# Optimization experiments

Hardware: AMD Instinct MI355X
Metric: run time of the kernel (lower is better)

Reference implementation:

```python
import jax, jax.numpy as jnp
import numpy as np
from jax import lax

KERNEL = 3      # patch size
STRIDE = 1      # matching stride at low res
RATE = 2        # downsample rate
SOFTMAX_SCALE = 10.0


def _extract_patches(img, k, stride):
    """tf.image.extract_patches with SAME padding. img: [B,H,W,C] -> [B, oh*ow, k, k, C]."""
    B, H, W, C = img.shape
    oh = -(-H // stride)
    ow = -(-W // stride)
    ph = max((oh - 1) * stride + k - H, 0)
    pw = max((ow - 1) * stride + k - W, 0)
    img = jnp.pad(img, ((0, 0), (ph // 2, ph - ph // 2), (pw // 2, pw - pw // 2), (0, 0)))
    # stack the k*k shifted strided views; channel-last order matches TF's (kh, kw, C) flattening
    cols = [img[:, dh:dh + (oh - 1) * stride + 1:stride, dw:dw + (ow - 1) * stride + 1:stride, :]
            for dh in range(k) for dw in range(k)]
    p = jnp.stack(cols, axis=3)  # [B, oh, ow, k*k, C]
    return p.reshape(B, oh * ow, k, k, C)


def _avgpool2(x):
    """Exact equivalent of TF bilinear (antialias=False) downsample by factor 2."""
    B, H, W, C = x.shape
    return x.reshape(B, H // 2, 2, W // 2, 2, C).mean(axis=(2, 4))


def _conv_same(x4, w):
    return lax.conv_general_dilated(x4, w, (1, 1), 'SAME',
                                    dimension_numbers=('NHWC', 'HWIO', 'NHWC'))


def _forward(x, mask):
    B, H, W, C = x.shape
    k, stride, rate = KERNEL, STRIDE, RATE
    h, w = H // rate, W // rate
    L = h * w

    # raw (full-res) patches used for reconstruction: [B,k,k,C,L]
    raw_w = jnp.transpose(_extract_patches(x, k, rate * stride), (0, 2, 3, 4, 1))
    # low-res foreground / background (identical here, as in the source)
    f = _avgpool2(x)              # [B,h,w,C]
    m = _avgpool2(mask)           # [B,h,w,1]
    # low-res matching patches: [B,k,k,C,L]
    wp = jnp.transpose(_extract_patches(f, k, stride), (0, 2, 3, 4, 1))
    # mask patches -> gate: mm = 1 where the 3x3 mask patch mean is exactly 1.0
    mp = _extract_patches(m, k, stride)                       # [B,L,k,k,1]
    mm = (jnp.mean(mp, axis=(2, 3, 4)) == 1.0).astype(jnp.float32)  # [B,L]

    fuse_w = jnp.eye(KERNEL, dtype=jnp.float32).reshape(KERNEL, KERNEL, 1, 1)

    def per_item(xi, wi, rwi, mmi):
        # xi:[h,w,C]  wi,rwi:[k,k,C,L]  mmi:[L]
        wn = wi / jnp.maximum(jnp.sqrt(jnp.sum(wi * wi, axis=(0, 1, 2))), 1e-4)
        yi = _conv_same(xi[None], wn)          # [1,h,w,L] cosine-similarity logits
        att = yi[0]
        # fuse: diagonal conv over the [L,L] score matrix in both patch orderings
        z = yi.reshape(1, L, L, 1)
        z = _conv_same(z, fuse_w)
        z = z.reshape(1, h, w, h, w).transpose(0, 2, 1, 4, 3).reshape(1, L, L, 1)
        z = _conv_same(z, fuse_w)
        z = z.reshape(1, w, h, w, h).transpose(0, 2, 1, 4, 3)
        yi = z.reshape(1, h, w, L)
        mm4 = mmi.reshape(1, 1, 1, L)
        yi = jax.nn.softmax(yi * mm4 * SOFTMAX_SCALE, axis=3) * mm4
        # reconstruction: transposed conv with raw full-res patches as filters
        out = lax.conv_transpose(yi, rwi, (rate, rate), 'SAME',
                                 dimension_numbers=('NHWC', 'HWIO', 'NHWC'),
                                 transpose_kernel=True) / float(rate * rate)
        return out[0], att

    y, att = jax.vmap(per_item)(f, wp, raw_w, mm)
    return y, att


def setup_inputs() -> dict:
    key = jax.random.key(0)
    x = jax.random.normal(key, (2, 128, 128, 64), dtype=jnp.float32)
    # binary hole mask: ones inside a centered 64x64 square
    mask = jnp.zeros((2, 128, 128, 1), jnp.float32).at[:, 32:96, 32:96, :].set(1.0)
    return {"x": x, "mask": mask}


def reference(x, mask):
    return _forward(x, mask)
```

## Files before the change

### kernel.cpp

```cpp
#include <hip/hip_runtime.h>
#include <hip/hip_bf16.h>

typedef _Float16 f16x8 __attribute__((ext_vector_type(8)));
typedef float f32x4 __attribute__((ext_vector_type(4)));

__device__ __forceinline__ void gload_lds16(const void* gptr, void* lptr) {
  __builtin_amdgcn_global_load_lds(
      (const __attribute__((address_space(1))) void*)gptr,
      (__attribute__((address_space(3))) void*)lptr, 16, 0, 0);
}

__global__ __launch_bounds__(256) void k_prt(const float* __restrict__ x,
                                             const float* __restrict__ mask,
                                             _Float16* __restrict__ f_h,
                                             float* __restrict__ sumsq,
                                             float* __restrict__ mlow,
                                             _Float16* __restrict__ Rt,
                                             float* __restrict__ y) {
  if (blockIdx.x < 2048) {
    int wave = threadIdx.x >> 6, c = threadIdx.x & 63;
    int blk = blockIdx.x * 4 + wave;
    int b = blk >> 12, ij = blk & 4095;
    int i = ij >> 6, j = ij & 63;
    size_t base = ((size_t)(b * 128 + 2 * i) * 128 + 2 * j) * 64 + c;
    float f = 0.25f * (x[base] + x[base + 64] + x[base + 128 * 64] + x[base + 128 * 64 + 64]);
    f_h[(size_t)blk * 64 + c] = (_Float16)f;
    float fsq = f * f;
    for (int off = 32; off; off >>= 1) fsq += __shfl_down(fsq, off);
    if (c == 0) {
      sumsq[blk] = fsq;
      size_t mb = (size_t)(b * 128 + 2 * i) * 128 + 2 * j;
      mlow[blk] = 0.25f * (mask[mb] + mask[mb + 1] + mask[mb + 128] + mask[mb + 129]);
    }
    return;
  }
  if (blockIdx.x >= 2432) {
    int idx = blockIdx.x - 2432;
    f32x4* Y4 = (f32x4*)y;
    f32x4 z = {0.f, 0.f, 0.f, 0.f};
#pragma unroll
    for (int k = 0; k < 4; ++k) Y4[idx * 1024 + k * 256 + threadIdx.x] = z;
    return;
  }
  int idx = blockIdx.x - 2048;
  int kh = idx % 3;
  int rest = idx / 3;
  int li = rest & 63, b = rest >> 6;
  int r = 2 * li + kh;
  __shared__ float xrow[128 * 65];
  if (r < 128) {
    for (int t = threadIdx.x; t < 8192; t += 256) {
      int v = t >> 6, c = t & 63;
      xrow[v * 65 + c] = x[((size_t)(b * 128 + r) * 128 + v) * 64 + c];
    }
  }
  __syncthreads();
  for (int id2 = threadIdx.x; id2 < 12288; id2 += 256) {
    int lj = id2 & 63, rest2 = id2 >> 6;
    int c = rest2 & 63, kw = rest2 >> 6;
    int v = 2 * lj + kw;
    float val = (r < 128 && v < 128) ? xrow[v * 65 + c] : 0.f;
    int n = (kh * 3 + kw) * 64 + c;
    Rt[((size_t)b * 640 + n) * 4096 + li * 64 + lj] = (_Float16)val;
  }
}

__global__ __launch_bounds__(1024) void k_norm_compact(const float* __restrict__ sumsq,
                                                       const float* __restrict__ mlow,
                                                       float* __restrict__ invn,
                                                       int* __restrict__ actIdx,
                                                       int* __restrict__ nAct) {
  int b = blockIdx.x;
  int t = threadIdx.x;
  __shared__ unsigned char mmf[4096];
  for (int l = t; l < 4096; l += 1024) {
    int li = l >> 6, lj = l & 63;
    float s = 0.f;
    bool ok = true;
    for (int dh = -1; dh <= 1; ++dh)
      for (int dw = -1; dw <= 1; ++dw) {
        int ii = li + dh, jj = lj + dw;
        float mv = 0.f;
        if ((unsigned)ii < 64u && (unsigned)jj < 64u) {
          int idx = (b << 12) + ii * 64 + jj;
          s += sumsq[idx];
          mv = mlow[idx];
        }
        ok = ok && (mv == 1.0f);
      }
    invn[(b << 12) + l] = 1.0f / fmaxf(sqrtf(s), 1e-4f);
    mmf[l] = ok ? 1 : 0;
  }
  __syncthreads();
  int lane = t & 63, wv = t >> 6;
  __shared__ int wsum[16];
  __shared__ int sbase;
  if (t == 0) sbase = 0;
  __syncthreads();
  for (int chunk = 0; chunk < 4; ++chunk) {
    int l = chunk * 1024 + t;
    int flag = mmf[l] ? 1 : 0;
    unsigned long long m = __ballot(flag);
    int wpre = __popcll(m & ((1ull << lane) - 1ull));
    if (lane == 0) wsum[wv] = __popcll(m);
    __syncthreads();
    int off = sbase;
    for (int w2 = 0; w2 < wv; ++w2) off += wsum[w2];
    if (flag) {
      int pos = off + wpre;
      if (pos < 1024) actIdx[(b << 10) + pos] = l;
    }
    __syncthreads();
    if (t == 0) {
      int s2 = 0;
      for (int w2 = 0; w2 < 16; ++w2) s2 += wsum[w2];
      sbase += s2;
    }
    __syncthreads();
  }
  int total = sbase;
  if (t >= total) actIdx[(b << 10) + t] = 0;
  if (t == 0) nAct[b] = (total > 1024) ? 1024 : total;
}

__global__ __launch_bounds__(256) void k_psub(const _Float16* __restrict__ f_h,
                                              _Float16* __restrict__ P,
                                              const _Float16* __restrict__ Rt,
                                              const int* __restrict__ actIdx,
                                              _Float16* __restrict__ Rts) {
  if (blockIdx.x < 2048) {
    int wave = threadIdx.x >> 6, c = threadIdx.x & 63;
    int blk = blockIdx.x * 4 + wave;
    int b = blk >> 12, l = blk & 4095;
    int li = l >> 6, lj = l & 63;
    _Float16* dst = P + (size_t)blk * 576 + c;
#pragma unroll
    for (int kk = 0; kk < 9; ++kk) {
      int kh = kk / 3, kw = kk % 3;
      int ii = li + kh - 1, jj = lj + kw - 1;
      _Float16 v = (_Float16)0.f;
      if ((unsigned)ii < 64u && (unsigned)jj < 64u)
        v = f_h[((size_t)(b << 12) + ii * 64 + jj) * 64 + c];
      dst[kk * 64] = v;
    }
    return;
  }
  int idx = blockIdx.x - 2048;
  int n = idx % 640, b = idx / 640;
  const unsigned short* src = (const unsigned short*)(Rt + ((size_t)b * 640 + n) * 4096);
  _Float16* dst = Rts + ((size_t)b * 640 + n) * 1024;
  const int* aIdx = actIdx + (b << 10);
  int s0 = threadIdx.x * 4;
  unsigned long long v = (unsigned long long)src[aIdx[s0]] |
                         ((unsigned long long)src[aIdx[s0 + 1]] << 16) |
                         ((unsigned long long)src[aIdx[s0 + 2]] << 32) |
                         ((unsigned long long)src[aIdx[s0 + 3]] << 48);
  *(unsigned long long*)(dst + s0) = v;
}

__global__ __launch_bounds__(256) void k_gemm_sim(const _Float16* __restrict__ P,
                                                  const float* __restrict__ invn,
                                                  float* __restrict__ att) {
  int b = blockIdx.z;
  const _Float16* Ab = P + (size_t)b * 4096 * 576;
  int idx0 = blockIdx.x;
  int idx = (idx0 & 7) * 66 + (idx0 >> 3);
  int bj = (int)((sqrtf(8.f * (float)idx + 1.f) - 1.f) * 0.5f);
  while ((bj + 1) * (bj + 2) / 2 <= idx) ++bj;
  while (bj * (bj + 1) / 2 > idx) --bj;
  int bi = idx - bj * (bj + 1) / 2;
  int rowBase = bi * 128, colBase = bj * 128;
  bool diag = (bi == bj);

  __shared__ alignas(16) _Float16 As[128 * 64];
  __shared__ alignas(16) _Float16 Bs[128 * 64];
  __shared__ alignas(16) float tbuf[32][132];
  int tid = threadIdx.x, wave = tid >> 6, lane = tid & 63;
  int q = lane >> 4, rr = lane & 15;
  int wr = (wave >> 1) * 64, wc = (wave & 1) * 64;
  f32x4 acc[4][4] = {};
  for (int kt = 0; kt < 576; kt += 64) {
    __syncthreads();
#pragma unroll
    for (int t = 0; t < 4; ++t) {
      int chunk = t * 256 + wave * 64 + lane;
      int row = chunk >> 3;
      int kc = ((chunk & 7) ^ (row & 7)) * 8;
      gload_lds16(Ab + (size_t)(rowBase + row) * 576 + kt + kc,
                  As + (size_t)(t * 256 + wave * 64) * 8);
      if (!diag)
        gload_lds16(Ab + (size_t)(colBase + row) * 576 + kt + kc,
                    Bs + (size_t)(t * 256 + wave * 64) * 8);
    }
    __syncthreads();
    const _Float16* Bsrc = diag ? As : Bs;
#pragma unroll
    for (int ks = 0; ks < 2; ++ks) {
      f16x8 af[4], bf[4];
#pragma unroll
      for (int mi = 0; mi < 4; ++mi) {
        int r = wr + mi * 16 + rr;
        int ps = (ks * 4 + q) ^ (r & 7);
        af[mi] = *(const f16x8*)(As + r * 64 + ps * 8);
      }
#pragma unroll
      for (int ni = 0; ni < 4; ++ni) {
        int r = wc + ni * 16 + rr;
        int ps = (ks * 4 + q) ^ (r & 7);
        bf[ni] = *(const f16x8*)(Bsrc + r * 64 + ps * 8);
      }
#pragma unroll
      for (int mi = 0; mi < 4; ++mi)
#pragma unroll
        for (int ni = 0; ni < 4; ++ni)
          acc[mi][ni] = __builtin_amdgcn_mfma_f32_16x16x32_f16(af[mi], bf[ni], acc[mi][ni], 0, 0, 0);
    }
  }
  float* attb = att + ((size_t)b << 24);
#pragma unroll
  for (int ni = 0; ni < 4; ++ni) {
    int gc = colBase + wc + ni * 16 + rr;
    float sc = invn[(b << 12) + gc];
#pragma unroll
    for (int mi = 0; mi < 4; ++mi)
#pragma unroll
      for (int reg = 0; reg < 4; ++reg) {
        int gr = rowBase + wr + mi * 16 + q * 4 + reg;
        attb[((size_t)gr << 12) + gc] = acc[mi][ni][reg] * sc;
      }
  }
  if (diag) return;
  const float* ivrow = invn + (b << 12) + rowBase;
#pragma unroll
  for (int ph = 0; ph < 4; ++ph) {
    __syncthreads();
    if ((ph >> 1) == (wc >> 6)) {
      int nlo = (ph & 1) * 2;
#pragma unroll
      for (int nn = 0; nn < 2; ++nn) {
        int ni = nlo + nn;
        int rloc = nn * 16 + rr;
#pragma unroll
        for (int mi = 0; mi < 4; ++mi)
          *(f32x4*)&tbuf[rloc][wr + mi * 16 + q * 4] = acc[mi][ni];
      }
    }
    __syncthreads();
    int r = tid >> 3;
    int cbase = (tid & 7) * 16;
    int grow = colBase + ph * 32 + r;
    float* dst = attb + ((size_t)grow << 12) + rowBase + cbase;
#pragma unroll
    for (int cc = 0; cc < 16; cc += 4) {
      f32x4 v = *(f32x4*)&tbuf[r][cbase + cc];
      f32x4 s = *(const f32x4*)(ivrow + cbase + cc);
      *(f32x4*)(dst + cc) = v * s;
    }
  }
}

__global__ __launch_bounds__(256) void k_fuse_softmax3(const float* __restrict__ att,
                                                       const int* __restrict__ actIdx,
                                                       const int* __restrict__ nAct,
                                                       _Float16* __restrict__ Asub) {
  int blk0 = blockIdx.x;
  int blk = (blk0 & 7) * 1024 + (blk0 >> 3);
  int b = blk >> 12, p = blk & 4095;
  const float* Y = att + ((size_t)b << 24);
  const int* aIdx = actIdx + (b << 10);
  int na = nAct[b];
  int tid = threadIdx.x;
  int pi = p >> 6, pj = p & 63;
  int acol = pj * 64 + pi;

  int ls[4];
  bool act[4];
  float F[4] = {0.f, 0.f, 0.f, 0.f};
#pragma unroll
  for (int s4 = 0; s4 < 4; ++s4) {
    int slot = s4 * 256 + tid;
    ls[s4] = aIdx[slot];
    act[s4] = (slot < na);
  }

#pragma unroll
  for (int d2 = -1; d2 <= 1; ++d2) {
    int a2 = acol + d2;
    if ((unsigned)a2 >= 4096u) continue;
    int p2 = ((a2 & 63) << 6) | (a2 >> 6);
    int l2[4];
    bool lok[4];
#pragma unroll
    for (int s4 = 0; s4 < 4; ++s4) {
      int l = ls[s4];
      int bcol = ((l & 63) << 6) | (l >> 6);
      int b2 = bcol + d2;
      lok[s4] = act[s4] && ((unsigned)b2 < 4096u);
      int b2c = lok[s4] ? b2 : 0;
      l2[s4] = ((b2c & 63) << 6) | (b2c >> 6);
    }
#pragma unroll
    for (int d1 = -1; d1 <= 1; ++d1) {
      int qq = p2 + d1;
      if ((unsigned)qq >= 4096u) continue;
      const float* row = Y + ((size_t)qq << 12);
#pragma unroll
      for (int s4 = 0; s4 < 4; ++s4) {
        int rr2 = l2[s4] + d1;
        if (lok[s4] && (unsigned)rr2 < 4096u) F[s4] += row[rr2];
      }
    }
  }

  float z[4];
  float mx = (na < 4096) ? 0.f : -1e30f;
#pragma unroll
  for (int s4 = 0; s4 < 4; ++s4) {
    z[s4] = act[s4] ? F[s4] * 10.f : -1e30f;
    mx = fmaxf(mx, z[s4]);
  }
  __shared__ float red[4];
  for (int off = 32; off; off >>= 1) mx = fmaxf(mx, __shfl_down(mx, off));
  if ((tid & 63) == 0) red[tid >> 6] = mx;
  __syncthreads();
  mx = fmaxf(fmaxf(red[0], red[1]), fmaxf(red[2], red[3]));
  float e[4];
  float esum = 0.f;
#pragma unroll
  for (int s4 = 0; s4 < 4; ++s4) {
    e[s4] = act[s4] ? __expf(z[s4] - mx) : 0.f;
    esum += e[s4];
  }
  for (int off = 32; off; off >>= 1) esum += __shfl_down(esum, off);
  __syncthreads();
  if ((tid & 63) == 0) red[tid >> 6] = esum;
  __syncthreads();
  float total = red[0] + red[1] + red[2] + red[3] + (float)(4096 - na) * __expf(0.f - mx);
  float inv = 1.f / total;
  _Float16* Ap = Asub + ((size_t)blk << 10);
#pragma unroll
  for (int s4 = 0; s4 < 4; ++s4) Ap[s4 * 256 + tid] = (_Float16)(e[s4] * inv);
}

__global__ __launch_bounds__(256) void k_gemm_recon(const _Float16* __restrict__ Asub,
                                                    const _Float16* __restrict__ Rts,
                                                    const int* __restrict__ nAct,
                                                    float* __restrict__ y) {
  int b = blockIdx.z;
  const _Float16* Ab = Asub + ((size_t)b << 22);
  const _Float16* Bb = Rts + (size_t)b * 640 * 1024;
  int kMax = ((nAct[b] + 63) >> 6) << 6;
  int rowBase = blockIdx.y * 128, colBase = blockIdx.x * 128;
  __shared__ alignas(16) _Float16 As[128 * 64];
  __shared__ alignas(16) _Float16 Bs[128 * 64];
  int tid = threadIdx.x, wave = tid >> 6, lane = tid & 63;
  int q = lane >> 4, rr = lane & 15;
  int wr = (wave >> 1) * 64, wc = (wave & 1) * 64;
  f32x4 acc[4][4] = {};
  for (int kt = 0; kt < kMax; kt += 64) {
    __syncthreads();
#pragma unroll
    for (int t = 0; t < 4; ++t) {
      int chunk = t * 256 + wave * 64 + lane;
      int row = chunk >> 3;
      int kc = ((chunk & 7) ^ (row & 7)) * 8;
      gload_lds16(Ab + ((size_t)(rowBase + row) << 10) + kt + kc,
                  As + (size_t)(t * 256 + wave * 64) * 8);
      gload_lds16(Bb + ((size_t)(colBase + row) << 10) + kt + kc,
                  Bs + (size_t)(t * 256 + wave * 64) * 8);
    }
    __syncthreads();
#pragma unroll
    for (int ks = 0; ks < 2; ++ks) {
      f16x8 af[4], bf[4];
#pragma unroll
      for (int mi = 0; mi < 4; ++mi) {
        int r = wr + mi * 16 + rr;
        int ps = (ks * 4 + q) ^ (r & 7);
        af[mi] = *(const f16x8*)(As + r * 64 + ps * 8);
      }
#pragma unroll
      for (int ni = 0; ni < 4; ++ni) {
        int r = wc + ni * 16 + rr;
        int ps = (ks * 4 + q) ^ (r & 7);
        bf[ni] = *(const f16x8*)(Bs + r * 64 + ps * 8);
      }
#pragma unroll
      for (int mi = 0; mi < 4; ++mi)
#pragma unroll
        for (int ni = 0; ni < 4; ++ni)
          acc[mi][ni] = __builtin_amdgcn_mfma_f32_16x16x32_f16(af[mi], bf[ni], acc[mi][ni], 0, 0, 0);
    }
  }
#pragma unroll
  for (int ni = 0; ni < 4; ++ni) {
    int gc = colBase + wc + ni * 16 + rr;
    if (gc < 576) {
      int kk = gc >> 6, c = gc & 63;
      int kh = kk / 3, kw = kk - kh * 3;
#pragma unroll
      for (int mi = 0; mi < 4; ++mi)
#pragma unroll
        for (int reg = 0; reg < 4; ++reg) {
          int gp = rowBase + wr + mi * 16 + q * 4 + reg;
          int i = gp >> 6, j = gp & 63;
          int u = 2 * i + kh, v = 2 * j + kw;
          if (u < 128 && v < 128)
            atomicAdd(y + (((size_t)((b * 128 + u) * 128 + v)) << 6) + c,
                      0.25f * acc[mi][ni][reg]);
        }
    }
  }
}

extern "C" void kernel_launch(void* const* d_in, const int* in_sizes, int n_in,
                              void* d_out, int out_size, void* d_ws, size_t ws_size,
                              hipStream_t stream) {
  const float* x = (const float*)d_in[0];
  const float* mask = (const float*)d_in[1];
  float* out = (float*)d_out;
  float* y = out;
  float* att = out + 2097152;

  char* ws = (char*)d_ws;
  _Float16* f_h = (_Float16*)(ws + 0);
  float* sumsq = (float*)(ws + 0x100000);
  float* mlow = (float*)(ws + 0x108000);
  float* invn = (float*)(ws + 0x110000);
  _Float16* P = (_Float16*)(ws + 0x120000);
  _Float16* Rt = (_Float16*)(ws + 0xA20000);
  int* actIdx = (int*)(ws + 0x1420000);
  int* nAct = (int*)(ws + 0x1422000);
  _Float16* Rts = (_Float16*)(ws + 0x1430000);
  _Float16* Asub = (_Float16*)(ws + 0x16B0000);
  (void)in_sizes; (void)n_in; (void)out_size; (void)ws_size;

  k_prt<<<2944, 256, 0, stream>>>(x, mask, f_h, sumsq, mlow, Rt, y);
  k_norm_compact<<<2, 1024, 0, stream>>>(sumsq, mlow, invn, actIdx, nAct);
  k_psub<<<3328, 256, 0, stream>>>(f_h, P, Rt, actIdx, Rts);
  k_gemm_sim<<<dim3(528, 1, 2), 256, 0, stream>>>(P, invn, att);
  k_fuse_softmax3<<<8192, 256, 0, stream>>>(att, actIdx, nAct, Asub);
  k_gemm_recon<<<dim3(5, 32, 2), 256, 0, stream>>>(Asub, Rts, nAct, y);
}
```

Baseline: 294.0 us.

## Gather raw patches directly from input and move norm computation into psub

Removes the full-size transposed raw-patch intermediate and instead gathers only the active patch columns directly from x when building the compacted reconstruction matrix. The inverse-norm computation is moved out of the two-block compaction kernel into extra parallel blocks of the gather kernel. This removes a large intermediate write and its read, at the cost of scattered, less coalesced reads from x.

```diff
diff --git a/kernel.cpp b/kernel.cpp
--- a/kernel.cpp
+++ b/kernel.cpp
@@ -15,7 +15,6 @@
                                              _Float16* __restrict__ f_h,
                                              float* __restrict__ sumsq,
                                              float* __restrict__ mlow,
-                                             _Float16* __restrict__ Rt,
                                              float* __restrict__ y) {
   if (blockIdx.x < 2048) {
     int wave = threadIdx.x >> 6, c = threadIdx.x & 63;
@@ -34,40 +33,14 @@
     }
     return;
   }
-  if (blockIdx.x >= 2432) {
-    int idx = blockIdx.x - 2432;
-    f32x4* Y4 = (f32x4*)y;
-    f32x4 z = {0.f, 0.f, 0.f, 0.f};
-#pragma unroll
-    for (int k = 0; k < 4; ++k) Y4[idx * 1024 + k * 256 + threadIdx.x] = z;
-    return;
-  }
   int idx = blockIdx.x - 2048;
-  int kh = idx % 3;
-  int rest = idx / 3;
-  int li = rest & 63, b = rest >> 6;
-  int r = 2 * li + kh;
-  __shared__ float xrow[128 * 65];
-  if (r < 128) {
-    for (int t = threadIdx.x; t < 8192; t += 256) {
-      int v = t >> 6, c = t & 63;
-      xrow[v * 65 + c] = x[((size_t)(b * 128 + r) * 128 + v) * 64 + c];
-    }
-  }
-  __syncthreads();
-  for (int id2 = threadIdx.x; id2 < 12288; id2 += 256) {
-    int lj = id2 & 63, rest2 = id2 >> 6;
-    int c = rest2 & 63, kw = rest2 >> 6;
-    int v = 2 * lj + kw;
-    float val = (r < 128 && v < 128) ? xrow[v * 65 + c] : 0.f;
-    int n = (kh * 3 + kw) * 64 + c;
-    Rt[((size_t)b * 640 + n) * 4096 + li * 64 + lj] = (_Float16)val;
-  }
-}
-
-__global__ __launch_bounds__(1024) void k_norm_compact(const float* __restrict__ sumsq,
-                                                       const float* __restrict__ mlow,
-                                                       float* __restrict__ invn,
+  f32x4* Y4 = (f32x4*)y;
+  f32x4 z = {0.f, 0.f, 0.f, 0.f};
+#pragma unroll
+  for (int k = 0; k < 4; ++k) Y4[idx * 1024 + k * 256 + threadIdx.x] = z;
+}
+
+__global__ __launch_bounds__(1024) void k_norm_compact(const float* __restrict__ mlow,
                                                        int* __restrict__ actIdx,
                                                        int* __restrict__ nAct) {
   int b = blockIdx.x;
@@ -75,20 +48,14 @@
   __shared__ unsigned char mmf[4096];
   for (int l = t; l < 4096; l += 1024) {
     int li = l >> 6, lj = l & 63;
-    float s = 0.f;
     bool ok = true;
     for (int dh = -1; dh <= 1; ++dh)
       for (int dw = -1; dw <= 1; ++dw) {
         int ii = li + dh, jj = lj + dw;
         float mv = 0.f;
-        if ((unsigned)ii < 64u && (unsigned)jj < 64u) {
-          int idx = (b << 12) + ii * 64 + jj;
-          s += sumsq[idx];
-          mv = mlow[idx];
-        }
+        if ((unsigned)ii < 64u && (unsigned)jj < 64u) mv = mlow[(b << 12) + ii * 64 + jj];
         ok = ok && (mv == 1.0f);
       }
-    invn[(b << 12) + l] = 1.0f / fmaxf(sqrtf(s), 1e-4f);
     mmf[l] = ok ? 1 : 0;
   }
   __syncthreads();
@@ -125,9 +92,11 @@
 
 __global__ __launch_bounds__(256) void k_psub(const _Float16* __restrict__ f_h,
                                               _Float16* __restrict__ P,
-                                              const _Float16* __restrict__ Rt,
+                                              const float* __restrict__ x,
                                               const int* __restrict__ actIdx,
-                                              _Float16* __restrict__ Rts) {
+                                              _Float16* __restrict__ Rts,
+                                              const float* __restrict__ sumsq,
+                                              float* __restrict__ invn) {
   if (blockIdx.x < 2048) {
     int wave = threadIdx.x >> 6, c = threadIdx.x & 63;
     int blk = blockIdx.x * 4 + wave;
@@ -145,16 +114,37 @@
     }
     return;
   }
+  if (blockIdx.x >= 3200) {
+    int t = (blockIdx.x - 3200) * 256 + threadIdx.x;
+    int b = t >> 12, l = t & 4095;
+    int li = l >> 6, lj = l & 63;
+    float s = 0.f;
+    for (int dh = -1; dh <= 1; ++dh)
+      for (int dw = -1; dw <= 1; ++dw) {
+        int ii = li + dh, jj = lj + dw;
+        if ((unsigned)ii < 64u && (unsigned)jj < 64u) s += sumsq[(b << 12) + ii * 64 + jj];
+      }
+    invn[t] = 1.0f / fmaxf(sqrtf(s), 1e-4f);
+    return;
+  }
   int idx = blockIdx.x - 2048;
-  int n = idx % 640, b = idx / 640;
-  const unsigned short* src = (const unsigned short*)(Rt + ((size_t)b * 640 + n) * 4096);
-  _Float16* dst = Rts + ((size_t)b * 640 + n) * 1024;
+  int n = idx % 576, b = idx / 576;
+  int kk = n >> 6, c = n & 63;
+  int kh = kk / 3, kw = kk - kh * 3;
+  _Float16* dst = Rts + ((size_t)(b * 640 + n) << 10);
   const int* aIdx = actIdx + (b << 10);
+  const float* xb = x + ((size_t)b << 20);
   int s0 = threadIdx.x * 4;
-  unsigned long long v = (unsigned long long)src[aIdx[s0]] |
-                         ((unsigned long long)src[aIdx[s0 + 1]] << 16) |
-                         ((unsigned long long)src[aIdx[s0 + 2]] << 32) |
-                         ((unsigned long long)src[aIdx[s0 + 3]] << 48);
+  unsigned long long v = 0;
+#pragma unroll
+  for (int u4 = 0; u4 < 4; ++u4) {
+    int l = aIdx[s0 + u4];
+    int li = l >> 6, lj = l & 63;
+    int r = 2 * li + kh, vv = 2 * lj + kw;
+    float val = (r < 128 && vv < 128) ? xb[((size_t)(r * 128 + vv) << 6) + c] : 0.f;
+    _Float16 h = (_Float16)val;
+    v |= ((unsigned long long)*(unsigned short*)&h) << (16 * u4);
+  }
   *(unsigned long long*)(dst + s0) = v;
 }
 
@@ -428,16 +418,15 @@
   float* mlow = (float*)(ws + 0x108000);
   float* invn = (float*)(ws + 0x110000);
   _Float16* P = (_Float16*)(ws + 0x120000);
-  _Float16* Rt = (_Float16*)(ws + 0xA20000);
   int* actIdx = (int*)(ws + 0x1420000);
   int* nAct = (int*)(ws + 0x1422000);
   _Float16* Rts = (_Float16*)(ws + 0x1430000);
   _Float16* Asub = (_Float16*)(ws + 0x16B0000);
   (void)in_sizes; (void)n_in; (void)out_size; (void)ws_size;
 
-  k_prt<<<2944, 256, 0, stream>>>(x, mask, f_h, sumsq, mlow, Rt, y);
-  k_norm_compact<<<2, 1024, 0, stream>>>(sumsq, mlow, invn, actIdx, nAct);
-  k_psub<<<3328, 256, 0, stream>>>(f_h, P, Rt, actIdx, Rts);
+  k_prt<<<2560, 256, 0, stream>>>(x, mask, f_h, sumsq, mlow, y);
+  k_norm_compact<<<2, 1024, 0, stream>>>(mlow, actIdx, nAct);
+  k_psub<<<3232, 256, 0, stream>>>(f_h, P, x, actIdx, Rts, sumsq, invn);
   k_gemm_sim<<<dim3(528, 1, 2), 256, 0, stream>>>(P, invn, att);
   k_fuse_softmax3<<<8192, 256, 0, stream>>>(att, actIdx, nAct, Asub);
   k_gemm_recon<<<dim3(5, 32, 2), 256, 0, stream>>>(Asub, Rts, nAct, y);
```

Result: faster. 285.4 us (-2.9%).
